# Performance work log

Hardware: AMD Instinct MI355X
Metric: run time of the kernel (lower is better)

## Reference

```python
import jax, jax.numpy as jnp
import numpy as np

J = 29  # joints per frame (from fc = Linear(29*3, 2))
C = 3   # feature channels (GCNConv(3, 3))


def setup_inputs() -> dict:
    key = jax.random.key(0)
    ks = jax.random.split(key, 6)
    batch_size, num_frames = 256, 1024
    n_total = batch_size * num_frames * J
    x = jax.random.normal(ks[0], (n_total, C), dtype=jnp.float32)
    edge_index = jax.random.randint(ks[1], (2, 56), 0, J, dtype=jnp.int64)
    # GCNConv(3,3) params and fc Linear(87,2) params
    W = jax.random.normal(ks[2], (C, C), dtype=jnp.float32) / np.sqrt(C)
    b = jnp.zeros((C,), dtype=jnp.float32)
    fc_W = jax.random.normal(ks[3], (J * C, 2), dtype=jnp.float32) / np.sqrt(J * C)
    fc_b = jnp.zeros((2,), dtype=jnp.float32)
    return {"x": x, "edge_index": edge_index, "batch_size": batch_size,
            "num_frames": num_frames, "W": W, "b": b, "fc_W": fc_W, "fc_b": fc_b}


def reference(x, edge_index, batch_size, num_frames, W, b, fc_W, fc_b):
    num_joints = x.shape[0] // (batch_size * num_frames)  # == J
    F = batch_size * num_frames
    self_idx = jnp.arange(num_joints, dtype=edge_index.dtype)
    src = jnp.concatenate([edge_index[0], self_idx])  # add self loops (PyG default)
    dst = jnp.concatenate([edge_index[1], self_idx])
    # symmetric degree normalization D^{-1/2}(A+I)D^{-1/2}
    deg = jnp.zeros((num_joints,), x.dtype).at[dst].add(1.0)
    dinv = jnp.where(deg > 0, jax.lax.rsqrt(deg), 0.0)
    norm = dinv[src] * dinv[dst]  # [E+J]
    # transform then aggregate, vectorized over all frames at once
    xw = (x @ W).reshape(F, num_joints, -1)  # [F, J, C]
    msgs = xw[:, src, :] * norm[None, :, None]  # [F, E+J, C]
    agg = jnp.zeros_like(xw).at[:, dst, :].add(msgs) + b  # scatter-add to targets
    h = jax.nn.relu(agg).reshape(batch_size, num_frames, num_joints * W.shape[1])
    h = jnp.mean(h, axis=1)  # [B, J*C] mean over frames
    z = jax.nn.sigmoid(h @ fc_W + fc_b)  # [B, 2]
    return (h, z)
```

## Files before the change

### kernel.cpp

```cpp
#include <hip/hip_runtime.h>
#include <math.h>

#define J   29
#define CH  3
#define JC  87
#define E0  56
#define B   256
#define T   1024
#define FRAMES (B*T)
#define FPC 64
#define CPB 4
#define NBLK (FRAMES/(FPC*CPB))
#define CHUNK_F4 1392
#define BPB (T/(FPC*CPB))
#define SLOTS 4
#define PROWS 32
#define MAXOV 96
#define WAVES 8
#define RPW 4

__global__ void prep_kernel(const int* __restrict__ ei,
                            int2* __restrict__ pairs,
                            int*  __restrict__ ov_rp,
                            int2* __restrict__ ov_pairs)
{
    __shared__ float M[J * J];
    __shared__ float dinv[J];
    __shared__ int   cnt_ov[J];
    int tid = threadIdx.x;

    for (int i = tid; i < J * J; i += 64) M[i] = 0.f;
    if (tid < J) {
        int d = 1;
        for (int e = 0; e < E0; ++e) d += (ei[E0 + e] == tid) ? 1 : 0;
        dinv[tid] = rsqrtf((float)d);
    }
    __syncthreads();

    if (tid < J) {
        for (int e = 0; e < E0; ++e) {
            if (ei[E0 + e] == tid) {
                int s = ei[e];
                M[tid * J + s] += dinv[s] * dinv[tid];
            }
        }
        M[tid * J + tid] += dinv[tid] * dinv[tid];
        int c = 0;
        for (int i = 0; i < J; ++i) c += (M[tid * J + i] != 0.f) ? 1 : 0;
        cnt_ov[tid] = (c > SLOTS) ? (c - SLOTS) : 0;
    }
    __syncthreads();

    if (tid == 0) {
        int a = 0;
        for (int j = 0; j < J; ++j) { ov_rp[j] = a; a += cnt_ov[j]; }
        for (int j = J; j <= 32; ++j) ov_rp[j] = a;
    }
    __syncthreads();

    if (tid < PROWS) {
        int2 zero; zero.x = 0; zero.y = 0;
        if (tid < J) {
            int s = 0, p = ov_rp[tid];
            for (int i = 0; i < J; ++i) {
                float v = M[tid * J + i];
                if (v != 0.f) {
                    if (s < SLOTS) {
                        int2 pr; pr.x = i * 12; pr.y = __float_as_int(v);
                        pairs[tid * SLOTS + s] = pr;
                    } else {
                        int2 pr; pr.x = (tid << 16) | (i * 12); pr.y = __float_as_int(v);
                        ov_pairs[p++] = pr;
                    }
                    ++s;
                }
            }
            for (; s < SLOTS; ++s) pairs[tid * SLOTS + s] = zero;
        } else {
            for (int s = 0; s < SLOTS; ++s) pairs[tid * SLOTS + s] = zero;
        }
    }
    __syncthreads();
    if (tid == 0) {
        int a = ov_rp[J];
        for (int i = a; i < MAXOV; ++i) { int2 pr; pr.x = 0; pr.y = 0; ov_pairs[i] = pr; }
    }
}

__global__ __launch_bounds__(512, 2)
void gcn_main(const float* __restrict__ x,
              const float* __restrict__ Wp,
              const float* __restrict__ bp,
              const int2* __restrict__ pairs,
              const int*  __restrict__ ov_rp,
              const int2* __restrict__ ov_pairs,
              float* __restrict__ partials) {
    __shared__ float4 xs4[2][CHUNK_F4];
    __shared__ int2   s_ov[MAXOV];

    int tid  = threadIdx.x;
    int lane = tid & 63;
    int wv   = tid >> 6;
    int rowbase = __builtin_amdgcn_readfirstlane(wv * RPW);

    float sW[9], sb[CH];
#pragma unroll
    for (int i = 0; i < 9; ++i) sW[i] = Wp[i];
#pragma unroll
    for (int i = 0; i < CH; ++i) sb[i] = bp[i];
    int ov0 = ov_rp[rowbase], ov1 = ov_rp[rowbase + RPW];
    if (tid < MAXOV) s_ov[tid] = ov_pairs[tid];

    const float4* src4 = (const float4*)x + (size_t)blockIdx.x * (CPB * CHUNK_F4);
    int i2 = 1024 + tid; if (i2 > CHUNK_F4 - 1) i2 = CHUNK_F4 - 1;

    float4 pfA0 = src4[tid], pfA1 = src4[512 + tid], pfA2 = src4[i2];
    const float4* s1 = src4 + CHUNK_F4;
    float4 pfB0 = s1[tid], pfB1 = s1[512 + tid], pfB2 = s1[i2];

    float acc[RPW][CH];
#pragma unroll
    for (int r = 0; r < RPW; ++r)
#pragma unroll
        for (int c = 0; c < CH; ++c) acc[r][c] = 0.f;

#define COMPUTE_CHUNK(BUF)                                                    \
    {                                                                         \
        const char* xf = (const char*)xs4[BUF] + lane * 348;                  \
        float y[RPW][CH];                                                     \
        _Pragma("unroll")                                                     \
        for (int R = 0; R < RPW; ++R) {                                       \
            float a0 = 0.f, a1 = 0.f, a2 = 0.f;                               \
            _Pragma("unroll")                                                 \
            for (int sl = 0; sl < SLOTS; ++sl) {                              \
                int2 pr = pairs[(rowbase + R) * SLOTS + sl];                  \
                float v = __int_as_float(pr.y);                               \
                const float* q = (const float*)(xf + pr.x);                   \
                a0 += v * q[0]; a1 += v * q[1]; a2 += v * q[2];               \
            }                                                                 \
            y[R][0] = a0; y[R][1] = a1; y[R][2] = a2;                         \
        }                                                                     \
        for (int e = ov0; e < ov1; ++e) {                                     \
            int2 pr = s_ov[e];                                                \
            int row = pr.x >> 16; int off = pr.x & 0xFFFF;                    \
            float v = __int_as_float(pr.y);                                   \
            const float* q = (const float*)(xf + off);                        \
            float d0 = v * q[0], d1 = v * q[1], d2 = v * q[2];                \
            _Pragma("unroll")                                                 \
            for (int R = 0; R < RPW; ++R)                                     \
                if (row == rowbase + R) { y[R][0] += d0; y[R][1] += d1; y[R][2] += d2; } \
        }                                                                     \
        _Pragma("unroll")                                                     \
        for (int R = 0; R < RPW; ++R)                                         \
            _Pragma("unroll")                                                 \
            for (int ch = 0; ch < CH; ++ch) {                                 \
                float t = y[R][0] * sW[0 * CH + ch]                           \
                        + y[R][1] * sW[1 * CH + ch]                           \
                        + y[R][2] * sW[2 * CH + ch]                           \
                        + sb[ch];                                             \
                acc[R][ch] += fmaxf(t, 0.f);                                  \
            }                                                                 \
    }

#define RAW_BARRIER()                                                         \
    asm volatile("s_waitcnt lgkmcnt(0)" ::: "memory");                        \
    __builtin_amdgcn_s_barrier();                                             \
    __builtin_amdgcn_sched_barrier(0);                                        \
    asm volatile("" ::: "memory");

#pragma unroll
    for (int c = 0; c < CPB; c += 2) {
        xs4[0][tid] = pfA0; xs4[0][512 + tid] = pfA1; xs4[0][i2] = pfA2;
        if (c + 2 < CPB) {
            const float4* sn = src4 + (c + 2) * CHUNK_F4;
            pfA0 = sn[tid]; pfA1 = sn[512 + tid]; pfA2 = sn[i2];
        }
        RAW_BARRIER();
        COMPUTE_CHUNK(0);

        xs4[1][tid] = pfB0; xs4[1][512 + tid] = pfB1; xs4[1][i2] = pfB2;
        if (c + 3 < CPB) {
            const float4* sn = src4 + (c + 3) * CHUNK_F4;
            pfB0 = sn[tid]; pfB1 = sn[512 + tid]; pfB2 = sn[i2];
        }
        RAW_BARRIER();
        COMPUTE_CHUNK(1);
    }

    __syncthreads();
    float* red = (float*)xs4[0];
#pragma unroll
    for (int R = 0; R < RPW; ++R) {
        int j = rowbase + R;
        if (j < J) {
#pragma unroll
            for (int ch = 0; ch < CH; ++ch)
                red[lane * JC + j * CH + ch] = acc[R][ch];
        }
    }
    __syncthreads();
    if (tid < JC) {
        float a = 0.f;
#pragma unroll
        for (int L = 0; L < FPC; ++L) a += red[L * JC + tid];
        partials[(size_t)blockIdx.x * JC + tid] = a;
    }
}

__global__ void finalize_kernel(const float* __restrict__ partials,
                                const float* __restrict__ fcW,
                                const float* __restrict__ fcb,
                                float* __restrict__ out) {
    __shared__ float h[JC];
    int b = blockIdx.x, tid = threadIdx.x;
    if (tid < JC) {
        float a = 0.f;
#pragma unroll
        for (int p = 0; p < BPB; ++p)
            a += partials[(size_t)(b * BPB + p) * JC + tid];
        a *= (1.0f / (float)T);
        h[tid] = a;
        out[(size_t)b * JC + tid] = a;
    }
    __syncthreads();
    if (tid < 2) {
        float a = fcb[tid];
        for (int r = 0; r < JC; ++r) a += h[r] * fcW[r * 2 + tid];
        out[(size_t)B * JC + b * 2 + tid] = 1.0f / (1.0f + expf(-a));
    }
}

extern "C" void kernel_launch(void* const* d_in, const int* in_sizes, int n_in,
                              void* d_out, int out_size, void* d_ws, size_t ws_size,
                              hipStream_t stream) {
    const float* x   = (const float*)d_in[0];
    const int*   ei  = (const int*)d_in[1];
    const float* W   = (const float*)d_in[4];
    const float* bb  = (const float*)d_in[5];
    const float* fcW = (const float*)d_in[6];
    const float* fcb = (const float*)d_in[7];

    char* ws = (char*)d_ws;
    int2* pairs    = (int2*)ws;
    int2* ov_pairs = pairs + PROWS * SLOTS;
    int*  ov_rp    = (int*)(ov_pairs + MAXOV);
    float* partials = (float*)(ws + 4096);

    prep_kernel<<<1, 64, 0, stream>>>(ei, pairs, ov_rp, ov_pairs);
    gcn_main<<<NBLK, WAVES * 64, 0, stream>>>(x, W, bb, pairs, ov_rp, ov_pairs, partials);
    finalize_kernel<<<B, 128, 0, stream>>>(partials, fcW, fcb, (float*)d_out);
}
```

Baseline: 42.54 us.

## Deepen load pipeline to three register sets and four LDS buffers, double chunks per block

Each block now processes eight chunks instead of four, halving the number of blocks. The loop is replaced by an explicit schedule with three register prefetch sets and four shared-memory buffers, so global loads run further ahead of compute. This aims to hide more memory latency and amortise per-block setup, at the cost of more LDS (about 89 KB per block) and registers, with occupancy pinned at two waves per EU and fewer blocks for the tail.

```diff
diff --git a/kernel.cpp b/kernel.cpp
--- a/kernel.cpp
+++ b/kernel.cpp
@@ -9,7 +9,7 @@
 #define T   1024
 #define FRAMES (B*T)
 #define FPC 64
-#define CPB 4
+#define CPB 8
 #define NBLK (FRAMES/(FPC*CPB))
 #define CHUNK_F4 1392
 #define BPB (T/(FPC*CPB))
@@ -87,7 +87,8 @@
     }
 }
 
-__global__ __launch_bounds__(512, 2)
+__global__ __launch_bounds__(512)
+__attribute__((amdgpu_waves_per_eu(2, 2)))
 void gcn_main(const float* __restrict__ x,
               const float* __restrict__ Wp,
               const float* __restrict__ bp,
@@ -95,7 +96,7 @@
               const int*  __restrict__ ov_rp,
               const int2* __restrict__ ov_pairs,
               float* __restrict__ partials) {
-    __shared__ float4 xs4[2][CHUNK_F4];
+    __shared__ float4 xs4[4][CHUNK_F4];
     __shared__ int2   s_ov[MAXOV];
 
     int tid  = threadIdx.x;
@@ -114,15 +115,25 @@
     const float4* src4 = (const float4*)x + (size_t)blockIdx.x * (CPB * CHUNK_F4);
     int i2 = 1024 + tid; if (i2 > CHUNK_F4 - 1) i2 = CHUNK_F4 - 1;
 
-    float4 pfA0 = src4[tid], pfA1 = src4[512 + tid], pfA2 = src4[i2];
-    const float4* s1 = src4 + CHUNK_F4;
-    float4 pfB0 = s1[tid], pfB1 = s1[512 + tid], pfB2 = s1[i2];
-
     float acc[RPW][CH];
 #pragma unroll
     for (int r = 0; r < RPW; ++r)
 #pragma unroll
         for (int c = 0; c < CH; ++c) acc[r][c] = 0.f;
+
+#define LOADSET(S, CK)                                                        \
+    {                                                                         \
+        const float4* sp_ = src4 + (CK) * CHUNK_F4;                           \
+        S##0 = sp_[tid]; S##1 = sp_[512 + tid]; S##2 = sp_[i2];               \
+    }
+#define WRITESET(S, BUF)                                                      \
+    xs4[BUF][tid] = S##0; xs4[BUF][512 + tid] = S##1; xs4[BUF][i2] = S##2;
+
+#define RAW_BARRIER()                                                         \
+    asm volatile("s_waitcnt lgkmcnt(0)" ::: "memory");                        \
+    __builtin_amdgcn_s_barrier();                                             \
+    __builtin_amdgcn_sched_barrier(0);                                        \
+    asm volatile("" ::: "memory");
 
 #define COMPUTE_CHUNK(BUF)                                                    \
     {                                                                         \
@@ -162,30 +173,20 @@
             }                                                                 \
     }
 
-#define RAW_BARRIER()                                                         \
-    asm volatile("s_waitcnt lgkmcnt(0)" ::: "memory");                        \
-    __builtin_amdgcn_s_barrier();                                             \
-    __builtin_amdgcn_sched_barrier(0);                                        \
-    asm volatile("" ::: "memory");
-
-#pragma unroll
-    for (int c = 0; c < CPB; c += 2) {
-        xs4[0][tid] = pfA0; xs4[0][512 + tid] = pfA1; xs4[0][i2] = pfA2;
-        if (c + 2 < CPB) {
-            const float4* sn = src4 + (c + 2) * CHUNK_F4;
-            pfA0 = sn[tid]; pfA1 = sn[512 + tid]; pfA2 = sn[i2];
-        }
-        RAW_BARRIER();
-        COMPUTE_CHUNK(0);
-
-        xs4[1][tid] = pfB0; xs4[1][512 + tid] = pfB1; xs4[1][i2] = pfB2;
-        if (c + 3 < CPB) {
-            const float4* sn = src4 + (c + 3) * CHUNK_F4;
-            pfB0 = sn[tid]; pfB1 = sn[512 + tid]; pfB2 = sn[i2];
-        }
-        RAW_BARRIER();
-        COMPUTE_CHUNK(1);
-    }
+    float4 SA0, SA1, SA2, SB0, SB1, SB2, SC0, SC1, SC2;
+
+    LOADSET(SA, 0)
+    LOADSET(SB, 1)
+    LOADSET(SC, 2)
+
+    WRITESET(SA, 0)  LOADSET(SA, 3)  RAW_BARRIER()  COMPUTE_CHUNK(0)
+    WRITESET(SB, 1)  LOADSET(SB, 4)  RAW_BARRIER()  COMPUTE_CHUNK(1)
+    WRITESET(SC, 2)  LOADSET(SC, 5)  RAW_BARRIER()  COMPUTE_CHUNK(2)
+    WRITESET(SA, 3)  LOADSET(SA, 6)  RAW_BARRIER()  COMPUTE_CHUNK(3)
+    WRITESET(SB, 0)  LOADSET(SB, 7)  RAW_BARRIER()  COMPUTE_CHUNK(0)
+    WRITESET(SC, 1)                  RAW_BARRIER()  COMPUTE_CHUNK(1)
+    WRITESET(SA, 2)                  RAW_BARRIER()  COMPUTE_CHUNK(2)
+    WRITESET(SB, 3)                  RAW_BARRIER()  COMPUTE_CHUNK(3)
 
     __syncthreads();
     float* red = (float*)xs4[0];
```

Measured after the change: 46.96 us. +10.4%, slower.
